# Performance work log

Measured on AMD Instinct MI355X. Metric: run time of the kernel, lower is better.

The kernel has to match this reference:

```python
import jax, jax.numpy as jnp
import numpy as np

N, E = 50000, 800000          # nodes, edges
D_EMB, D_HID = 64, 64          # n_embed, n_hidden


def setup_inputs() -> dict:
    key = jax.random.key(0)
    k0, k1, k2, k3 = jax.random.split(key, 4)
    prop_edge_index = jax.random.randint(k0, (2, E), 0, N, dtype=jnp.int32)
    emb = jax.random.normal(k1, (N, D_EMB), dtype=jnp.float32)          # embedding.weight
    W1 = jax.random.normal(k2, (D_EMB, D_HID), dtype=jnp.float32) / np.float32(np.sqrt(D_EMB))
    b1 = jnp.zeros((D_HID,), jnp.float32)
    W2 = jax.random.normal(k3, (D_HID, D_HID), dtype=jnp.float32) / np.float32(np.sqrt(D_HID))
    b2 = jnp.zeros((D_HID,), jnp.float32)
    return {"prop_edge_index": prop_edge_index, "emb": emb,
            "W1": W1, "b1": b1, "W2": W2, "b2": b2}


def _gcn_conv(x, W, b, src, dst, n):
    """PyG GCNConv: D^{-1/2}(A+I)D^{-1/2} (x @ W) + b, aggregation at dst."""
    h = x @ W                                                   # [N, D]
    deg = jax.ops.segment_sum(jnp.ones_like(dst, jnp.float32), dst,
                              num_segments=n) + 1.0             # +1 self-loop
    dinv = jax.lax.rsqrt(deg)                                   # [N]
    coef = dinv[src] * dinv[dst]                                # [E]
    msg = h[src] * coef[:, None]                                # [E, D] gather
    agg = jax.ops.segment_sum(msg, dst, num_segments=n)         # scatter-add
    agg = agg + h * (dinv * dinv)[:, None]                      # self-loop term
    return agg + b


def reference(prop_edge_index, emb, W1, b1, W2, b2):
    src, dst = prop_edge_index[0], prop_edge_index[1]
    x = jax.nn.relu(_gcn_conv(emb, W1, b1, src, dst, N))
    # dropout is identity at inference (args.training = False)
    return _gcn_conv(x, W2, b2, src, dst, N)
```

## Files before the change

### kernel.cpp

```cpp
#include <hip/hip_runtime.h>
#include <hip/hip_fp16.h>

#define D 64
#define KMAX 64

__global__ __launch_bounds__(256) void k_zero(int* __restrict__ p, int n4) {
    int stride = gridDim.x * blockDim.x;
    for (int i = blockIdx.x * blockDim.x + threadIdx.x; i < n4; i += stride)
        reinterpret_cast<int4*>(p)[i] = make_int4(0, 0, 0, 0);
}

__global__ __launch_bounds__(256) void k_fill_gemm(
    const int* __restrict__ src, const int* __restrict__ dst,
    int* __restrict__ cnt, int* __restrict__ csr, int e, int n,
    const float* __restrict__ X, const float* __restrict__ W,
    __half* __restrict__ G, int ntiles, int fill_blocks) {
    __shared__ float Ws[D][D];
    __shared__ float Xs[16][D + 4];

    if (blockIdx.x < fill_blocks) {
        int r = blockIdx.x & 7;
        int lo = (int)(((long long)r * n) >> 3);
        int hi = (int)(((long long)(r + 1) * n) >> 3);
        int nch = fill_blocks >> 3;
        int chunk = blockIdx.x >> 3;
        for (int i = chunk * blockDim.x + threadIdx.x; i < e; i += nch * blockDim.x) {
            int d = dst[i];
            if (d >= lo && d < hi) {
                int pos = atomicAdd(&cnt[d], 1);
                csr[(d << 6) + pos] = src[i];
            }
        }
        return;
    }

    int tid = threadIdx.x;
    int rl = tid >> 4;
    int c4 = tid & 15;
    int gb = blockIdx.x - fill_blocks;
    int ngb = gridDim.x - fill_blocks;

    for (int i = tid; i < (D * D) / 4; i += 256)
        reinterpret_cast<float4*>(&Ws[0][0])[i] = reinterpret_cast<const float4*>(W)[i];

    for (int tile = gb; tile < ntiles; tile += ngb) {
        int row = tile * 16 + rl;
        __syncthreads();
        {
            float4 v = make_float4(0.f, 0.f, 0.f, 0.f);
            if (row < n) v = reinterpret_cast<const float4*>(X)[(size_t)row * 16 + c4];
            *reinterpret_cast<float4*>(&Xs[rl][c4 * 4]) = v;
        }
        __syncthreads();

        float4 acc = make_float4(0.f, 0.f, 0.f, 0.f);
#pragma unroll
        for (int k = 0; k < D; ++k) {
            float xk = Xs[rl][k];
            float4 w = *reinterpret_cast<const float4*>(&Ws[k][c4 * 4]);
            acc.x += xk * w.x; acc.y += xk * w.y;
            acc.z += xk * w.z; acc.w += xk * w.w;
        }
        if (row < n) {
            __half2 h01 = __floats2half2_rn(acc.x, acc.y);
            __half2 h23 = __floats2half2_rn(acc.z, acc.w);
            int2 packed;
            packed.x = *reinterpret_cast<int*>(&h01);
            packed.y = *reinterpret_cast<int*>(&h23);
            reinterpret_cast<int2*>(G)[(size_t)row * 16 + c4] = packed;
        }
    }
}

template <bool RELU>
__global__ __launch_bounds__(256) void k_agg(const __half* __restrict__ G,
                                             const int* __restrict__ cnt,
                                             const int* __restrict__ csr,
                                             const float* __restrict__ bias,
                                             float* __restrict__ out, int n) {
    int wid = (blockIdx.x * blockDim.x + threadIdx.x) >> 6;
    if (wid >= n) return;
    int lane = threadIdx.x & 63;
    int eq = lane >> 4;
    int c4 = lane & 15;
    int deg = cnt[wid];
    const int4* bucket = reinterpret_cast<const int4*>(csr + (wid << 6));

    float4 acc = make_float4(0.f, 0.f, 0.f, 0.f);
    for (int q = eq; q * 4 < deg; q += 4) {
        int4 sv = bucket[q];
        int nvalid = deg - q * 4;
        int sidx[4] = {sv.x, sv.y, sv.z, sv.w};
#pragma unroll
        for (int j = 0; j < 4; ++j) {
            bool v = (j < nvalid);
            int s = v ? sidx[j] : 0;
            float ds = v ? rsqrtf((float)(cnt[s] + 1)) : 0.f;
            int2 raw = reinterpret_cast<const int2*>(G)[(size_t)s * 16 + c4];
            __half2 p0 = *reinterpret_cast<__half2*>(&raw.x);
            __half2 p1 = *reinterpret_cast<__half2*>(&raw.y);
            float2 f0 = __half22float2(p0);
            float2 f1 = __half22float2(p1);
            acc.x += ds * f0.x; acc.y += ds * f0.y;
            acc.z += ds * f1.x; acc.w += ds * f1.y;
        }
    }
#pragma unroll
    for (int off = 16; off < 64; off <<= 1) {
        acc.x += __shfl_xor(acc.x, off);
        acc.y += __shfl_xor(acc.y, off);
        acc.z += __shfl_xor(acc.z, off);
        acc.w += __shfl_xor(acc.w, off);
    }
    if (eq == 0) {
        float dv = rsqrtf((float)(deg + 1));
        int2 raw = reinterpret_cast<const int2*>(G)[(size_t)wid * 16 + c4];
        __half2 p0 = *reinterpret_cast<__half2*>(&raw.x);
        __half2 p1 = *reinterpret_cast<__half2*>(&raw.y);
        float2 f0 = __half22float2(p0);
        float2 f1 = __half22float2(p1);
        float4 b4 = reinterpret_cast<const float4*>(bias)[c4];
        float4 o;
        o.x = (acc.x + dv * f0.x) * dv + b4.x;
        o.y = (acc.y + dv * f0.y) * dv + b4.y;
        o.z = (acc.z + dv * f1.x) * dv + b4.z;
        o.w = (acc.w + dv * f1.y) * dv + b4.w;
        if (RELU) {
            o.x = fmaxf(o.x, 0.f); o.y = fmaxf(o.y, 0.f);
            o.z = fmaxf(o.z, 0.f); o.w = fmaxf(o.w, 0.f);
        }
        reinterpret_cast<float4*>(out)[(size_t)wid * 16 + c4] = o;
    }
}

__global__ __launch_bounds__(256, 4) void k_gemm2b(const float* __restrict__ X,
                                                   const float* __restrict__ W,
                                                   __half* __restrict__ G, int n, int ntiles) {
    __shared__ float Ws[D][D];
    __shared__ float Xs[32][D];
    int tid = threadIdx.x;
    int col = tid & 63;
    int rq = tid >> 6;

    for (int i = tid; i < (D * D) / 4; i += 256)
        reinterpret_cast<float4*>(&Ws[0][0])[i] = reinterpret_cast<const float4*>(W)[i];

    for (int tile = blockIdx.x; tile < ntiles; tile += gridDim.x) {
        int rowbase = tile * 32;
        __syncthreads();
        if (rowbase + 32 <= n) {
            const float4* xp = reinterpret_cast<const float4*>(X + (size_t)rowbase * D);
            for (int i = tid; i < (32 * D) / 4; i += 256)
                reinterpret_cast<float4*>(&Xs[0][0])[i] = xp[i];
        } else {
            for (int i = tid; i < 32 * D; i += 256) {
                int r = rowbase + (i >> 6);
                Xs[i >> 6][i & 63] = (r < n) ? X[(size_t)r * D + (i & 63)] : 0.f;
            }
        }
        __syncthreads();

        float acc[8];
#pragma unroll
        for (int j = 0; j < 8; ++j) acc[j] = 0.f;
#pragma unroll 4
        for (int k4 = 0; k4 < D; k4 += 4) {
            float w0 = Ws[k4 + 0][col];
            float w1 = Ws[k4 + 1][col];
            float w2 = Ws[k4 + 2][col];
            float w3 = Ws[k4 + 3][col];
#pragma unroll
            for (int j = 0; j < 8; ++j) {
                float4 xv = *reinterpret_cast<const float4*>(&Xs[(rq << 3) + j][k4]);
                acc[j] += xv.x * w0 + xv.y * w1 + xv.z * w2 + xv.w * w3;
            }
        }
#pragma unroll
        for (int j = 0; j < 8; ++j) {
            int r = rowbase + (rq << 3) + j;
            if (r < n) G[(size_t)r * D + col] = __float2half(acc[j]);
        }
    }
}


extern "C" void kernel_launch(void* const* d_in, const int* in_sizes, int n_in,
                              void* d_out, int out_size, void* d_ws, size_t ws_size,
                              hipStream_t stream) {
    const int* ei = (const int*)d_in[0];
    const float* emb = (const float*)d_in[1];
    const float* W1 = (const float*)d_in[2];
    const float* b1 = (const float*)d_in[3];
    const float* W2 = (const float*)d_in[4];
    const float* b2 = (const float*)d_in[5];
    float* out = (float*)d_out;

    int E = in_sizes[0] / 2;
    int N = in_sizes[1] / D;
    const int* src = ei;
    const int* dst = ei + E;

    auto al = [](size_t v) { return (v + 255) & ~(size_t)255; };
    char* ws = (char*)d_ws;
    size_t off = 0;
    int* cnt = (int*)(ws + off);      off = al(off + (size_t)N * 4);
    int* csr = (int*)(ws + off);      off = al(off + (size_t)N * KMAX * 4);
    __half* g1 = (__half*)(ws + off); off = al(off + (size_t)N * D * 2);
    float* x = (float*)(ws + off);    off = al(off + (size_t)N * D * 4);
    __half* g2 = (__half*)(ws + off); off = al(off + (size_t)N * D * 2);

    int ntiles16 = (N + 15) / 16;
    int ntiles32 = (N + 31) / 32;
    int fill_blocks = 1024;
    int gemm_blocks = 512;
    int row_blocks = (N + 3) / 4;

    hipLaunchKernelGGL(k_zero, dim3(512), dim3(256), 0, stream, cnt, (N + 3) / 4);
    hipLaunchKernelGGL(k_fill_gemm, dim3(fill_blocks + gemm_blocks), dim3(256), 0, stream,
                       src, dst, cnt, csr, E, N, emb, W1, g1, ntiles16, fill_blocks);
    hipLaunchKernelGGL(k_agg<true>, dim3(row_blocks), dim3(256), 0, stream,
                       g1, cnt, csr, b1, x, N);
    hipLaunchKernelGGL(k_gemm2b, dim3(1024), dim3(256), 0, stream,
                       x, W2, g2, N, ntiles32);
    hipLaunchKernelGGL(k_agg<false>, dim3(row_blocks), dim3(256), 0, stream,
                       g2, cnt, csr, b2, out, N);
}
```

Baseline: 129.1 us.

## Store hidden activations in fp16 and pre-scale layer-2 features by source dinv

The layer-1 aggregation now writes the ReLU output as fp16 instead of fp32, halving the intermediate write and the read in the second GEMM. The second GEMM multiplies each output row by its rsqrt degree, so the layer-2 aggregation no longer has to gather cnt[s] and compute rsqrt per edge. The cost is fp16 rounding of the hidden layer and one extra cnt read per row in the GEMM epilogue.

```diff
diff --git a/kernel.cpp b/kernel.cpp
--- a/kernel.cpp
+++ b/kernel.cpp
@@ -72,12 +72,11 @@
     }
 }
 
-template <bool RELU>
-__global__ __launch_bounds__(256) void k_agg(const __half* __restrict__ G,
-                                             const int* __restrict__ cnt,
-                                             const int* __restrict__ csr,
-                                             const float* __restrict__ bias,
-                                             float* __restrict__ out, int n) {
+__global__ __launch_bounds__(256) void k_agg1(const __half* __restrict__ G,
+                                              const int* __restrict__ cnt,
+                                              const int* __restrict__ csr,
+                                              const float* __restrict__ bias,
+                                              __half* __restrict__ x, int n) {
     int wid = (blockIdx.x * blockDim.x + threadIdx.x) >> 6;
     if (wid >= n) return;
     int lane = threadIdx.x & 63;
@@ -120,21 +119,22 @@
         float2 f0 = __half22float2(p0);
         float2 f1 = __half22float2(p1);
         float4 b4 = reinterpret_cast<const float4*>(bias)[c4];
-        float4 o;
-        o.x = (acc.x + dv * f0.x) * dv + b4.x;
-        o.y = (acc.y + dv * f0.y) * dv + b4.y;
-        o.z = (acc.z + dv * f1.x) * dv + b4.z;
-        o.w = (acc.w + dv * f1.y) * dv + b4.w;
-        if (RELU) {
-            o.x = fmaxf(o.x, 0.f); o.y = fmaxf(o.y, 0.f);
-            o.z = fmaxf(o.z, 0.f); o.w = fmaxf(o.w, 0.f);
-        }
-        reinterpret_cast<float4*>(out)[(size_t)wid * 16 + c4] = o;
-    }
-}
-
-__global__ __launch_bounds__(256, 4) void k_gemm2b(const float* __restrict__ X,
+        float ox = fmaxf((acc.x + dv * f0.x) * dv + b4.x, 0.f);
+        float oy = fmaxf((acc.y + dv * f0.y) * dv + b4.y, 0.f);
+        float oz = fmaxf((acc.z + dv * f1.x) * dv + b4.z, 0.f);
+        float ow = fmaxf((acc.w + dv * f1.y) * dv + b4.w, 0.f);
+        __half2 h01 = __floats2half2_rn(ox, oy);
+        __half2 h23 = __floats2half2_rn(oz, ow);
+        int2 packed;
+        packed.x = *reinterpret_cast<int*>(&h01);
+        packed.y = *reinterpret_cast<int*>(&h23);
+        reinterpret_cast<int2*>(x)[(size_t)wid * 16 + c4] = packed;
+    }
+}
+
+__global__ __launch_bounds__(256, 4) void k_gemm2b(const __half* __restrict__ X,
                                                    const float* __restrict__ W,
+                                                   const int* __restrict__ cnt,
                                                    __half* __restrict__ G, int n, int ntiles) {
     __shared__ float Ws[D][D];
     __shared__ float Xs[32][D];
@@ -148,15 +148,19 @@
     for (int tile = blockIdx.x; tile < ntiles; tile += gridDim.x) {
         int rowbase = tile * 32;
         __syncthreads();
-        if (rowbase + 32 <= n) {
-            const float4* xp = reinterpret_cast<const float4*>(X + (size_t)rowbase * D);
-            for (int i = tid; i < (32 * D) / 4; i += 256)
-                reinterpret_cast<float4*>(&Xs[0][0])[i] = xp[i];
-        } else {
-            for (int i = tid; i < 32 * D; i += 256) {
-                int r = rowbase + (i >> 6);
-                Xs[i >> 6][i & 63] = (r < n) ? X[(size_t)r * D + (i & 63)] : 0.f;
-            }
+        for (int i = tid; i < 32 * 16; i += 256) {
+            int rr = rowbase + (i >> 4);
+            int p = i & 15;
+            float4 f = make_float4(0.f, 0.f, 0.f, 0.f);
+            if (rr < n) {
+                int2 raw = reinterpret_cast<const int2*>(X)[(size_t)rr * 16 + p];
+                __half2 h0 = *reinterpret_cast<__half2*>(&raw.x);
+                __half2 h1 = *reinterpret_cast<__half2*>(&raw.y);
+                float2 f0 = __half22float2(h0);
+                float2 f1 = __half22float2(h1);
+                f = make_float4(f0.x, f0.y, f1.x, f1.y);
+            }
+            *reinterpret_cast<float4*>(&Xs[i >> 4][p * 4]) = f;
         }
         __syncthreads();
 
@@ -178,8 +182,67 @@
 #pragma unroll
         for (int j = 0; j < 8; ++j) {
             int r = rowbase + (rq << 3) + j;
-            if (r < n) G[(size_t)r * D + col] = __float2half(acc[j]);
-        }
+            if (r < n) {
+                float dv = rsqrtf((float)(cnt[r] + 1));
+                G[(size_t)r * D + col] = __float2half(acc[j] * dv);
+            }
+        }
+    }
+}
+
+__global__ __launch_bounds__(256) void k_agg2(const __half* __restrict__ G,
+                                              const int* __restrict__ cnt,
+                                              const int* __restrict__ csr,
+                                              const float* __restrict__ bias,
+                                              float* __restrict__ out, int n) {
+    int wid = (blockIdx.x * blockDim.x + threadIdx.x) >> 6;
+    if (wid >= n) return;
+    int lane = threadIdx.x & 63;
+    int eq = lane >> 4;
+    int c4 = lane & 15;
+    int deg = cnt[wid];
+    const int4* bucket = reinterpret_cast<const int4*>(csr + (wid << 6));
+
+    float4 acc = make_float4(0.f, 0.f, 0.f, 0.f);
+    for (int q = eq; q * 4 < deg; q += 4) {
+        int4 sv = bucket[q];
+        int nvalid = deg - q * 4;
+        int sidx[4] = {sv.x, sv.y, sv.z, sv.w};
+#pragma unroll
+        for (int j = 0; j < 4; ++j) {
+            bool v = (j < nvalid);
+            int s = v ? sidx[j] : 0;
+            float wgt = v ? 1.f : 0.f;
+            int2 raw = reinterpret_cast<const int2*>(G)[(size_t)s * 16 + c4];
+            __half2 p0 = *reinterpret_cast<__half2*>(&raw.x);
+            __half2 p1 = *reinterpret_cast<__half2*>(&raw.y);
+            float2 f0 = __half22float2(p0);
+            float2 f1 = __half22float2(p1);
+            acc.x += wgt * f0.x; acc.y += wgt * f0.y;
+            acc.z += wgt * f1.x; acc.w += wgt * f1.y;
+        }
+    }
+#pragma unroll
+    for (int off = 16; off < 64; off <<= 1) {
+        acc.x += __shfl_xor(acc.x, off);
+        acc.y += __shfl_xor(acc.y, off);
+        acc.z += __shfl_xor(acc.z, off);
+        acc.w += __shfl_xor(acc.w, off);
+    }
+    if (eq == 0) {
+        float dv = rsqrtf((float)(deg + 1));
+        int2 raw = reinterpret_cast<const int2*>(G)[(size_t)wid * 16 + c4];
+        __half2 p0 = *reinterpret_cast<__half2*>(&raw.x);
+        __half2 p1 = *reinterpret_cast<__half2*>(&raw.y);
+        float2 f0 = __half22float2(p0);
+        float2 f1 = __half22float2(p1);
+        float4 b4 = reinterpret_cast<const float4*>(bias)[c4];
+        float4 o;
+        o.x = (acc.x + f0.x) * dv + b4.x;
+        o.y = (acc.y + f0.y) * dv + b4.y;
+        o.z = (acc.z + f1.x) * dv + b4.z;
+        o.w = (acc.w + f1.y) * dv + b4.w;
+        reinterpret_cast<float4*>(out)[(size_t)wid * 16 + c4] = o;
     }
 }
 
@@ -206,7 +269,7 @@
     int* cnt = (int*)(ws + off);      off = al(off + (size_t)N * 4);
     int* csr = (int*)(ws + off);      off = al(off + (size_t)N * KMAX * 4);
     __half* g1 = (__half*)(ws + off); off = al(off + (size_t)N * D * 2);
-    float* x = (float*)(ws + off);    off = al(off + (size_t)N * D * 4);
+    __half* x = (__half*)(ws + off);  off = al(off + (size_t)N * D * 2);
     __half* g2 = (__half*)(ws + off); off = al(off + (size_t)N * D * 2);
 
     int ntiles16 = (N + 15) / 16;
@@ -218,10 +281,10 @@
     hipLaunchKernelGGL(k_zero, dim3(512), dim3(256), 0, stream, cnt, (N + 3) / 4);
     hipLaunchKernelGGL(k_fill_gemm, dim3(fill_blocks + gemm_blocks), dim3(256), 0, stream,
                        src, dst, cnt, csr, E, N, emb, W1, g1, ntiles16, fill_blocks);
-    hipLaunchKernelGGL(k_agg<true>, dim3(row_blocks), dim3(256), 0, stream,
+    hipLaunchKernelGGL(k_agg1, dim3(row_blocks), dim3(256), 0, stream,
                        g1, cnt, csr, b1, x, N);
     hipLaunchKernelGGL(k_gemm2b, dim3(1024), dim3(256), 0, stream,
-                       x, W2, g2, N, ntiles32);
-    hipLaunchKernelGGL(k_agg<false>, dim3(row_blocks), dim3(256), 0, stream,
+                       x, W2, cnt, g2, N, ntiles32);
+    hipLaunchKernelGGL(k_agg2, dim3(row_blocks), dim3(256), 0, stream,
                        g2, cnt, csr, b2, out, N);
 }
```

New measurement: 120.4 us. -6.7%, faster.
